# Performance work log

Hardware: AMD Instinct MI355X
Metric: run time of the kernel (lower is better)

Reference implementation:

```python
import jax, jax.numpy as jnp
import numpy as np

MARGIN = 0.3
N = 8192
D = 128
NUM_CLASSES = 256

def setup_inputs() -> dict:
    key = jax.random.key(0)
    k1, k2 = jax.random.split(key)
    inputs = jax.random.normal(k1, (N, D), dtype=jnp.float32)
    targets = jax.random.randint(k2, (N,), 0, NUM_CLASSES, dtype=jnp.int64)
    return {"inputs": inputs, "targets": targets}

def reference(inputs, targets):
    n = inputs.shape[0]
    dt = inputs.dtype
    # pairwise euclidean distances: ||xi||^2 + ||xj||^2 - 2 xi.xj, clamped and sqrt'ed
    sq = jnp.sum(inputs * inputs, axis=1)                     # [n]
    d2 = sq[:, None] + sq[None, :] - 2.0 * (inputs @ inputs.T)
    dist = jnp.sqrt(jnp.clip(d2, 1e-12, None))                # [n, n]
    dsq = dist * dist                                         # squared dists used by the loss

    mask = targets[:, None] == targets[None, :]               # same-identity mask [n, n]

    # positives: torch code sorts and drops the smallest (the self-distance ~1e-6)
    pos_d = jnp.where(mask, dist, jnp.inf)
    min_idx = jnp.argmin(pos_d, axis=1)                       # index of dropped element per row
    excl = jnp.arange(n)[None, :] == min_idx[:, None]
    pos_valid = mask & ~excl                                  # remaining positives
    cnt_p = jnp.sum(pos_valid, axis=1).astype(dt)
    sigma_p = jnp.sum(jnp.where(pos_valid, dsq, 0.0), axis=1) / cnt_p
    max_p = jnp.max(jnp.where(pos_valid, dsq, -jnp.inf), axis=1)
    dist_ap = max_p / sigma_p + 0.5 * jnp.log(sigma_p)        # [n]

    # negatives: all different-identity entries
    neg = ~mask
    cnt_n = jnp.sum(neg, axis=1).astype(dt)
    sigma_n = jnp.sum(jnp.where(neg, dsq, 0.0), axis=1) / cnt_n
    min_n = jnp.min(jnp.where(neg, dsq, jnp.inf), axis=1)
    dist_an = min_n / sigma_n + 0.5 * jnp.log(sigma_n)        # [n]

    # MarginRankingLoss with y=1: mean(max(0, -(an - ap) + margin))
    loss = jnp.mean(jnp.maximum(dist_ap - dist_an + MARGIN, 0.0))
    return loss
```

## Files before the change

kernel.cpp:

```cpp
#include <hip/hip_runtime.h>
#include <math.h>


#define NROWS 8192
#define MARGIN_F 0.3f

#define OFF_SQ   0
#define OFF_UPK  8192
#define OFF_XBF  16384
#define OFF_PART 540672

typedef short bf16x8 __attribute__((ext_vector_type(8)));
typedef float f32x16 __attribute__((ext_vector_type(16)));
union U4B { uint4 u; bf16x8 h; };

__device__ __forceinline__ unsigned short f2bf(float x) {
    unsigned u = __float_as_uint(x);
    return (unsigned short)((u + 0x7fffu + ((u >> 16) & 1u)) >> 16);
}

__global__ __launch_bounds__(256) void prep_kernel(const float* __restrict__ X,
                                                   const int* __restrict__ tgt,
                                                   float* __restrict__ sq,
                                                   float* __restrict__ upk,
                                                   unsigned short* __restrict__ Xbf,
                                                   float* __restrict__ out) {
    int tid = threadIdx.x, w = tid >> 6, l = tid & 63;
    #pragma unroll
    for (int i = 0; i < 4; ++i) {
        int r = blockIdx.x * 16 + w * 4 + i;
        float2 v = ((const float2*)X)[(size_t)r * 64 + l];
        ushort2 h2;
        h2.x = f2bf(v.x);
        h2.y = f2bf(v.y);
        ((ushort2*)Xbf)[(size_t)r * 64 + l] = h2;
        float s = v.x * v.x + v.y * v.y;
        for (int d = 32; d > 0; d >>= 1) s += __shfl_down(s, d, 64);
        if (l == 0) {
            sq[r] = s;
            upk[r] = __uint_as_float((__float_as_uint(0.5f * s) & 0xffffff00u)
                                     | (unsigned)tgt[r]);
        }
    }
    if (blockIdx.x == 0 && tid == 0) out[0] = 0.0f;
}

__global__ __launch_bounds__(256, 4) void dist_kernel(
        const unsigned short* __restrict__ Xbf, const int* __restrict__ tgt,
        const float* __restrict__ upk, float4* __restrict__ partial,
        int ns_mask, int jb_shift, int tiles) {
    __shared__ uint4 As[128 * 16];
    __shared__ float ush[128];
    const int tid = threadIdx.x;
    const int w = tid >> 6, l = tid & 63, hl = l >> 5, l31 = l & 31;
    const int bx = blockIdx.x;
    const int slice = bx & ns_mask;
    const int jb = bx >> jb_shift;

    {
        const uint4* src = (const uint4*)Xbf + (size_t)jb * 64 * 16;
        #pragma unroll
        for (int s = 0; s < 4; ++s) {
            int g = s * 256 + tid, row = g >> 4, c = g & 15;
            As[row * 16 + (c ^ (row & 15))] = src[g];
        }
    }
    __syncthreads();
    bf16x8 Bf[2][8];
    int tjt[2];
    #pragma unroll
    for (int ct = 0; ct < 2; ++ct) {
        int colb = ct * 32 + l31;
        tjt[ct] = tgt[jb * 64 + colb];
        #pragma unroll
        for (int kk = 0; kk < 8; ++kk) {
            U4B t; t.u = As[colb * 16 + ((kk * 2 + hl) ^ (colb & 15))];
            Bf[ct][kk] = t.h;
        }
    }

    float Sa[2] = {0.f, 0.f};
    float Ss[2] = {0.f, 0.f};
    float Mp[2] = {-INFINITY, -INFINITY};
    float Mn[2] = { INFINITY,  INFINITY};

    for (int t = 0; t < tiles; ++t) {
        const int i0 = (slice * tiles + t) * 128;
        __syncthreads();
        {
            const uint4* src = (const uint4*)Xbf + (size_t)i0 * 16;
            #pragma unroll
            for (int s = 0; s < 8; ++s) {
                int g = s * 256 + tid, row = g >> 4, c = g & 15;
                As[row * 16 + (c ^ (row & 15))] = src[g];
            }
            if (tid < 128) ush[tid] = upk[i0 + tid];
        }
        __syncthreads();

        float ur[16];
        int tags[16];
        #pragma unroll
        for (int r = 0; r < 16; ++r) {
            ur[r] = ush[w * 32 + (r & 3) + 8 * (r >> 2) + 4 * hl];
            tags[r] = __float_as_int(ur[r]) & 0xff;
        }

        f32x16 acc[2];
        acc[0] = (f32x16)0.0f;
        acc[1] = (f32x16)0.0f;
        const int arow = w * 32 + l31;
        #pragma unroll
        for (int kk = 0; kk < 8; ++kk) {
            U4B a; a.u = As[arow * 16 + ((kk * 2 + hl) ^ (arow & 15))];
            acc[0] = __builtin_amdgcn_mfma_f32_32x32x16_bf16(a.h, Bf[0][kk], acc[0], 0, 0, 0);
            acc[1] = __builtin_amdgcn_mfma_f32_32x32x16_bf16(a.h, Bf[1][kk], acc[1], 0, 0, 0);
        }

        #pragma unroll
        for (int ct = 0; ct < 2; ++ct) {
            const int tt = tjt[ct];
            #pragma unroll
            for (int r = 0; r < 16; ++r) {
                float a = acc[ct][r];
                float v = ur[r] - a;
                bool same = (tags[r] == tt);
                Sa[ct] += a;
                Ss[ct] += same ? a : 0.0f;
                Mp[ct] = fmaxf(Mp[ct], same ? v : -INFINITY);
                Mn[ct] = same ? Mn[ct] : fminf(Mn[ct], v);
            }
        }
    }

    #pragma unroll
    for (int ct = 0; ct < 2; ++ct) {
        Sa[ct] += __shfl_xor(Sa[ct], 32, 64);
        Ss[ct] += __shfl_xor(Ss[ct], 32, 64);
        Mp[ct] = fmaxf(Mp[ct], __shfl_xor(Mp[ct], 32, 64));
        Mn[ct] = fminf(Mn[ct], __shfl_xor(Mn[ct], 32, 64));
    }
    __syncthreads();
    float4* sm = (float4*)As;
    if (l < 32) {
        #pragma unroll
        for (int ct = 0; ct < 2; ++ct)
            sm[(ct * 32 + l31) * 4 + w] = make_float4(Sa[ct], Ss[ct], Mp[ct], Mn[ct]);
    }
    __syncthreads();
    if (tid < 64) {
        float4 a = sm[tid * 4 + 0], b = sm[tid * 4 + 1];
        float4 c2 = sm[tid * 4 + 2], d = sm[tid * 4 + 3];
        float4 o;
        o.x = a.x + b.x + c2.x + d.x;
        o.y = a.y + b.y + c2.y + d.y;
        o.z = fmaxf(fmaxf(a.z, b.z), fmaxf(c2.z, d.z));
        o.w = fminf(fminf(a.w, b.w), fminf(c2.w, d.w));
        partial[(size_t)slice * NROWS + jb * 64 + tid] = o;
    }
}

__global__ __launch_bounds__(256) void combine_kernel(
        const int* __restrict__ tgt, const float* __restrict__ sq,
        const float4* __restrict__ partial, float* __restrict__ out, int ns) {
    __shared__ float scl[256];
    __shared__ int cnt[256];
    __shared__ float red[4];
    __shared__ float hs[4];
    int tid = threadIdx.x, w = tid >> 6, l = tid & 63;
    scl[tid] = 0.0f;
    cnt[tid] = 0;
    __syncthreads();
    for (int it = 0; it < 32; ++it) {
        int r = it * 256 + tid;
        int c = tgt[r];
        atomicAdd(&scl[c], sq[r]);
        atomicAdd(&cnt[c], 1);
    }
    __syncthreads();
    float s = scl[tid];
    for (int d = 32; d > 0; d >>= 1) s += __shfl_down(s, d, 64);
    if (l == 0) red[w] = s;
    __syncthreads();
    float S_all = red[0] + red[1] + red[2] + red[3];

    int j = blockIdx.x * 256 + tid;
    float Sa = 0.f, Ss = 0.f, Mp = -INFINITY, Mn = INFINITY;
    for (int s2 = 0; s2 < ns; ++s2) {
        float4 p = partial[(size_t)s2 * NROWS + j];
        Sa += p.x; Ss += p.y;
        Mp = fmaxf(Mp, p.z); Mn = fminf(Mn, p.w);
    }
    float sqj = sq[j];
    int c = tgt[j];
    float cm = (float)cnt[c];
    float sumall = (float)NROWS * sqj + S_all - 2.0f * Sa;
    float sump = cm * sqj + scl[c] - 2.0f * Ss;
    float sumn = sumall - sump;
    float sigp = sump / (cm - 1.0f);
    float sign_ = sumn / ((float)NROWS - cm);
    float ap = (sqj + 2.0f * Mp) / sigp + 0.5f * __logf(sigp);
    float an = (sqj + 2.0f * Mn) / sign_ + 0.5f * __logf(sign_);
    float h = fmaxf(ap - an + MARGIN_F, 0.0f);
    for (int d = 32; d > 0; d >>= 1) h += __shfl_down(h, d, 64);
    if (l == 0) hs[w] = h;
    __syncthreads();
    if (tid == 0)
        atomicAdd(out, (hs[0] + hs[1] + hs[2] + hs[3]) * (1.0f / NROWS));
}

extern "C" void kernel_launch(void* const* d_in, const int* in_sizes, int n_in,
                              void* d_out, int out_size, void* d_ws, size_t ws_size,
                              hipStream_t stream) {
    const float* X = (const float*)d_in[0];
    const int* tgt = (const int*)d_in[1];
    float* out = (float*)d_out;
    float* f = (float*)d_ws;

    float* sq  = f + OFF_SQ;
    float* upk = f + OFF_UPK;
    unsigned short* Xbf = (unsigned short*)(f + OFF_XBF);
    float4* partial = (float4*)(f + OFF_PART);

    int ns = 16;
    while (ns > 2 && ws_size < ((size_t)OFF_PART + (size_t)ns * NROWS * 4) * sizeof(float))
        ns >>= 1;
    int shift = (ns == 16) ? 4 : (ns == 8) ? 3 : 2;
    int tiles = 64 / ns;

    prep_kernel<<<512, 256, 0, stream>>>(X, tgt, sq, upk, Xbf, out);
    dist_kernel<<<128 * ns, 256, 0, stream>>>(Xbf, tgt, upk, partial,
                                              ns - 1, shift, tiles);
    combine_kernel<<<32, 256, 0, stream>>>(tgt, sq, partial, out, ns);
}
```

Measured before the change: 120.4 us.

## Sort rows by class and compute distance sums algebraically outside the GEMM loop

Rows are counting-sorted by class label, so same-class entries form a contiguous band. The per-row sums of squared distances are computed separately from class-sum and global-sum vectors via dot products. This leaves the GEMM epilogue doing only the positive max and negative min, with a cheap min-only path for tiles that contain no same-class rows. It adds four small kernels (histogram, prefix offsets, scatter, class dots) plus extra launches and serial per-class work in exchange for a lighter epilogue and smaller partial output.

New measurement: 135.4 us. +12.4%, slower.

```diff
diff --git a/kernel.cpp b/kernel.cpp
--- a/kernel.cpp
+++ b/kernel.cpp
@@ -5,10 +5,22 @@
 #define NROWS 8192
 #define MARGIN_F 0.3f
 
-#define OFF_SQ   0
-#define OFF_UPK  8192
-#define OFF_XBF  16384
-#define OFF_PART 540672
+#define O_HIST   0
+#define O_OFF    256
+#define O_BOFF   512
+#define O_BH     16896
+#define O_PCS    33280
+#define O_PSQ    41472
+#define O_SVEC   41536
+#define O_SALL   41664
+#define O_SQ     41680
+#define O_US     49872
+#define O_CSA    58064
+#define O_WDA    66256
+#define O_SUMP   74448
+#define O_SUMALL 82640
+#define O_XS     90832
+#define O_PART   615120
 
 typedef short bf16x8 __attribute__((ext_vector_type(8)));
 typedef float f32x16 __attribute__((ext_vector_type(16)));
@@ -18,39 +30,193 @@
     unsigned u = __float_as_uint(x);
     return (unsigned short)((u + 0x7fffu + ((u >> 16) & 1u)) >> 16);
 }
+__device__ __forceinline__ float b2f(unsigned short h) {
+    return __uint_as_float(((unsigned)h) << 16);
+}
 
 __global__ __launch_bounds__(256) void prep_kernel(const float* __restrict__ X,
                                                    const int* __restrict__ tgt,
-                                                   float* __restrict__ sq,
-                                                   float* __restrict__ upk,
-                                                   unsigned short* __restrict__ Xbf,
-                                                   float* __restrict__ out) {
-    int tid = threadIdx.x, w = tid >> 6, l = tid & 63;
-    #pragma unroll
-    for (int i = 0; i < 4; ++i) {
-        int r = blockIdx.x * 16 + w * 4 + i;
+                                                   float* __restrict__ f) {
+    int*   bh  = (int*)(f + O_BH);
+    float* pcs = f + O_PCS;
+    float* psq = f + O_PSQ;
+    float* sq  = f + O_SQ;
+    __shared__ int lh[256];
+    __shared__ float csum[128];
+    __shared__ float ph[4];
+    int tid = threadIdx.x, w = tid >> 6, l = tid & 63, b = blockIdx.x;
+    int row0 = b * 128;
+    lh[tid] = 0;
+    __syncthreads();
+    if (tid < 128) atomicAdd(&lh[tgt[row0 + tid]], 1);
+    {
+        int d = tid & 127, r0 = (tid >> 7) * 64;
+        float a = 0.0f;
+        #pragma unroll 8
+        for (int r = 0; r < 64; ++r)
+            a += X[(size_t)(row0 + r0 + r) * 128 + d];
+        if (tid < 128) csum[tid] = a;
+        __syncthreads();
+        if (tid >= 128) csum[tid - 128] += a;
+        __syncthreads();
+        if (tid < 128) pcs[b * 128 + tid] = csum[tid];
+    }
+    float ss = 0.0f;
+    for (int i = 0; i < 32; ++i) {
+        int r = row0 + w * 32 + i;
         float2 v = ((const float2*)X)[(size_t)r * 64 + l];
+        float s = v.x * v.x + v.y * v.y;
+        for (int d = 32; d > 0; d >>= 1) s += __shfl_down(s, d, 64);
+        if (l == 0) { sq[r] = s; ss += s; }
+    }
+    if (l == 0) ph[w] = ss;
+    __syncthreads();
+    if (tid == 0) psq[b] = ph[0] + ph[1] + ph[2] + ph[3];
+    bh[b * 256 + tid] = lh[tid];
+}
+
+__global__ __launch_bounds__(256) void offsets_kernel(float* __restrict__ f,
+                                                      float* __restrict__ out) {
+    int*   hist = (int*)(f + O_HIST);
+    int*   off  = (int*)(f + O_OFF);
+    int*   boff = (int*)(f + O_BOFF);
+    int*   bh   = (int*)(f + O_BH);
+    float* pcs  = f + O_PCS;
+    float* psq  = f + O_PSQ;
+    float* svec = f + O_SVEC;
+    float* sall = f + O_SALL;
+    __shared__ int sh[256];
+    int c = threadIdx.x;
+    int h = 0;
+    for (int b = 0; b < 64; ++b) h += bh[b * 256 + c];
+    hist[c] = h;
+    sh[c] = h;
+    __syncthreads();
+    for (int d = 1; d < 256; d <<= 1) {
+        int t = (c >= d) ? sh[c - d] : 0;
+        __syncthreads();
+        sh[c] += t;
+        __syncthreads();
+    }
+    int o = sh[c] - h;
+    off[c] = o;
+    int run = o;
+    for (int b = 0; b < 64; ++b) {
+        boff[b * 256 + c] = run;
+        run += bh[b * 256 + c];
+    }
+    if (c < 128) {
+        float s = 0.0f;
+        for (int b = 0; b < 64; ++b) s += pcs[b * 128 + c];
+        svec[c] = s;
+    }
+    if (c < 64) {
+        float t = psq[c];
+        for (int d = 32; d > 0; d >>= 1) t += __shfl_down(t, d, 64);
+        if (c == 0) sall[0] = t;
+    }
+    if (c == 0) out[0] = 0.0f;
+}
+
+__global__ __launch_bounds__(256) void scatter_kernel(const float* __restrict__ X,
+                                                      const int* __restrict__ tgt,
+                                                      float* __restrict__ f) {
+    int*   hist = (int*)(f + O_HIST);
+    int*   off  = (int*)(f + O_OFF);
+    int*   boff = (int*)(f + O_BOFF);
+    float* sq   = f + O_SQ;
+    float* u_s  = f + O_US;
+    int*   csA  = (int*)(f + O_CSA);
+    int*   wdA  = (int*)(f + O_WDA);
+    unsigned short* Xs = (unsigned short*)(f + O_XS);
+    __shared__ int cur[256];
+    __shared__ int pos_sh[128];
+    int tid = threadIdx.x, b = blockIdx.x;
+    cur[tid] = boff[b * 256 + tid];
+    __syncthreads();
+    int row0 = b * 128;
+    if (tid < 128) {
+        int c = tgt[row0 + tid];
+        int p = atomicAdd(&cur[c], 1);
+        pos_sh[tid] = p;
+        u_s[p] = 0.5f * sq[row0 + tid];
+        csA[p] = off[c];
+        wdA[p] = hist[c];
+    }
+    __syncthreads();
+    int w = tid >> 6, l = tid & 63;
+    #pragma unroll 4
+    for (int i = 0; i < 32; ++i) {
+        int rl = w * 32 + i;
+        int p = pos_sh[rl];
+        float2 v = ((const float2*)X)[(size_t)(row0 + rl) * 64 + l];
         ushort2 h2;
         h2.x = f2bf(v.x);
         h2.y = f2bf(v.y);
-        ((ushort2*)Xbf)[(size_t)r * 64 + l] = h2;
-        float s = v.x * v.x + v.y * v.y;
-        for (int d = 32; d > 0; d >>= 1) s += __shfl_down(s, d, 64);
+        ((ushort2*)Xs)[(size_t)p * 64 + l] = h2;
+    }
+}
+
+__global__ __launch_bounds__(256) void classdot_kernel(float* __restrict__ f) {
+    int*   hist = (int*)(f + O_HIST);
+    int*   off  = (int*)(f + O_OFF);
+    float* svg  = f + O_SVEC;
+    float* sall = f + O_SALL;
+    float* u_s  = f + O_US;
+    float* sump_s   = f + O_SUMP;
+    float* sumall_s = f + O_SUMALL;
+    unsigned short* Xs = (unsigned short*)(f + O_XS);
+    __shared__ float sv[128];
+    __shared__ float cv[128];
+    __shared__ float sclsh;
+    int c = blockIdx.x, tid = threadIdx.x, w = tid >> 6, l = tid & 63;
+    int n = hist[c], cs0 = off[c];
+    if (tid < 128) sv[tid] = svg[tid];
+    {
+        int d = tid & 127;
+        float a = 0.0f;
+        for (int k = (tid >> 7); k < n; k += 2)
+            a += b2f(Xs[(size_t)(cs0 + k) * 128 + d]);
+        if (tid < 128) cv[tid] = a;
+        __syncthreads();
+        if (tid >= 128) cv[tid - 128] += a;
+    }
+    if (tid == 0) {
+        float s = 0.0f;
+        for (int k = 0; k < n; ++k) s += 2.0f * u_s[cs0 + k];
+        sclsh = s;
+    }
+    __syncthreads();
+    float Scl = sclsh, SA = sall[0];
+    for (int k = w; k < n; k += 4) {
+        int j = cs0 + k;
+        ushort2 xv = ((const ushort2*)Xs)[(size_t)j * 64 + l];
+        float x0 = b2f(xv.x), x1 = b2f(xv.y);
+        float pa = sv[2 * l] * x0 + sv[2 * l + 1] * x1;
+        float pb = cv[2 * l] * x0 + cv[2 * l + 1] * x1;
+        for (int d = 32; d > 0; d >>= 1) {
+            pa += __shfl_down(pa, d, 64);
+            pb += __shfl_down(pb, d, 64);
+        }
         if (l == 0) {
-            sq[r] = s;
-            upk[r] = __uint_as_float((__float_as_uint(0.5f * s) & 0xffffff00u)
-                                     | (unsigned)tgt[r]);
-        }
-    }
-    if (blockIdx.x == 0 && tid == 0) out[0] = 0.0f;
-}
-
-__global__ __launch_bounds__(256, 4) void dist_kernel(
-        const unsigned short* __restrict__ Xbf, const int* __restrict__ tgt,
-        const float* __restrict__ upk, float4* __restrict__ partial,
-        int ns_mask, int jb_shift, int tiles) {
+            float sqj = 2.0f * u_s[j];
+            sump_s[j]   = (float)n * sqj + Scl - 2.0f * pb;
+            sumall_s[j] = (float)NROWS * sqj + SA - 2.0f * pa;
+        }
+    }
+}
+
+__global__ __launch_bounds__(256, 3) void dist_kernel(float* __restrict__ f,
+                                                      int ns_mask, int jb_shift,
+                                                      int tiles) {
     __shared__ uint4 As[128 * 16];
     __shared__ float ush[128];
+    float* u_s = f + O_US;
+    int*   csA = (int*)(f + O_CSA);
+    int*   wdA = (int*)(f + O_WDA);
+    unsigned short* Xs = (unsigned short*)(f + O_XS);
+    float2* partial = (float2*)(f + O_PART);
+
     const int tid = threadIdx.x;
     const int w = tid >> 6, l = tid & 63, hl = l >> 5, l31 = l & 31;
     const int bx = blockIdx.x;
@@ -58,7 +224,7 @@
     const int jb = bx >> jb_shift;
 
     {
-        const uint4* src = (const uint4*)Xbf + (size_t)jb * 64 * 16;
+        const uint4* src = (const uint4*)Xs + (size_t)jb * 64 * 16;
         #pragma unroll
         for (int s = 0; s < 4; ++s) {
             int g = s * 256 + tid, row = g >> 4, c = g & 15;
@@ -67,11 +233,12 @@
     }
     __syncthreads();
     bf16x8 Bf[2][8];
-    int tjt[2];
+    int cs[2], wd[2];
     #pragma unroll
     for (int ct = 0; ct < 2; ++ct) {
         int colb = ct * 32 + l31;
-        tjt[ct] = tgt[jb * 64 + colb];
+        cs[ct] = csA[jb * 64 + colb];
+        wd[ct] = wdA[jb * 64 + colb];
         #pragma unroll
         for (int kk = 0; kk < 8; ++kk) {
             U4B t; t.u = As[colb * 16 + ((kk * 2 + hl) ^ (colb & 15))];
@@ -79,8 +246,6 @@
         }
     }
 
-    float Sa[2] = {0.f, 0.f};
-    float Ss[2] = {0.f, 0.f};
     float Mp[2] = {-INFINITY, -INFINITY};
     float Mn[2] = { INFINITY,  INFINITY};
 
@@ -88,22 +253,25 @@
         const int i0 = (slice * tiles + t) * 128;
         __syncthreads();
         {
-            const uint4* src = (const uint4*)Xbf + (size_t)i0 * 16;
+            const uint4* src = (const uint4*)Xs + (size_t)i0 * 16;
             #pragma unroll
             for (int s = 0; s < 8; ++s) {
                 int g = s * 256 + tid, row = g >> 4, c = g & 15;
                 As[row * 16 + (c ^ (row & 15))] = src[g];
             }
-            if (tid < 128) ush[tid] = upk[i0 + tid];
+            if (tid < 128) ush[tid] = u_s[i0 + tid];
         }
         __syncthreads();
 
         float ur[16];
-        int tags[16];
-        #pragma unroll
-        for (int r = 0; r < 16; ++r) {
-            ur[r] = ush[w * 32 + (r & 3) + 8 * (r >> 2) + 4 * hl];
-            tags[r] = __float_as_int(ur[r]) & 0xff;
+        {
+            const int base = w * 32 + 4 * hl;
+            #pragma unroll
+            for (int q = 0; q < 4; ++q) {
+                float4 uq = *(const float4*)&ush[base + 8 * q];
+                ur[4 * q + 0] = uq.x; ur[4 * q + 1] = uq.y;
+                ur[4 * q + 2] = uq.z; ur[4 * q + 3] = uq.w;
+            }
         }
 
         f32x16 acc[2];
@@ -119,86 +287,74 @@
 
         #pragma unroll
         for (int ct = 0; ct < 2; ++ct) {
-            const int tt = tjt[ct];
-            #pragma unroll
-            for (int r = 0; r < 16; ++r) {
-                float a = acc[ct][r];
-                float v = ur[r] - a;
-                bool same = (tags[r] == tt);
-                Sa[ct] += a;
-                Ss[ct] += same ? a : 0.0f;
-                Mp[ct] = fmaxf(Mp[ct], same ? v : -INFINITY);
-                Mn[ct] = same ? Mn[ct] : fminf(Mn[ct], v);
+            bool band = (cs[ct] < i0 + 128) && (cs[ct] + wd[ct] > i0);
+            if (__any(band)) {
+                int rowb = i0 + w * 32 + 4 * hl - cs[ct];
+                unsigned wdu = (unsigned)wd[ct];
+                #pragma unroll
+                for (int r = 0; r < 16; ++r) {
+                    float v = ur[r] - acc[ct][r];
+                    bool in = (unsigned)(rowb + (r & 3) + 8 * (r >> 2)) < wdu;
+                    Mp[ct] = fmaxf(Mp[ct], in ? v : -INFINITY);
+                    Mn[ct] = in ? Mn[ct] : fminf(Mn[ct], v);
+                }
+            } else {
+                #pragma unroll
+                for (int r = 0; r < 16; r += 2) {
+                    float v1 = ur[r] - acc[ct][r];
+                    float v2 = ur[r + 1] - acc[ct][r + 1];
+                    Mn[ct] = fminf(Mn[ct], fminf(v1, v2));
+                }
             }
         }
     }
 
     #pragma unroll
     for (int ct = 0; ct < 2; ++ct) {
-        Sa[ct] += __shfl_xor(Sa[ct], 32, 64);
-        Ss[ct] += __shfl_xor(Ss[ct], 32, 64);
         Mp[ct] = fmaxf(Mp[ct], __shfl_xor(Mp[ct], 32, 64));
         Mn[ct] = fminf(Mn[ct], __shfl_xor(Mn[ct], 32, 64));
     }
     __syncthreads();
-    float4* sm = (float4*)As;
+    float2* sm = (float2*)As;
     if (l < 32) {
         #pragma unroll
         for (int ct = 0; ct < 2; ++ct)
-            sm[(ct * 32 + l31) * 4 + w] = make_float4(Sa[ct], Ss[ct], Mp[ct], Mn[ct]);
+            sm[(ct * 32 + l31) * 4 + w] = make_float2(Mp[ct], Mn[ct]);
     }
     __syncthreads();
     if (tid < 64) {
-        float4 a = sm[tid * 4 + 0], b = sm[tid * 4 + 1];
-        float4 c2 = sm[tid * 4 + 2], d = sm[tid * 4 + 3];
-        float4 o;
-        o.x = a.x + b.x + c2.x + d.x;
-        o.y = a.y + b.y + c2.y + d.y;
-        o.z = fmaxf(fmaxf(a.z, b.z), fmaxf(c2.z, d.z));
-        o.w = fminf(fminf(a.w, b.w), fminf(c2.w, d.w));
+        float2 a = sm[tid * 4 + 0], b = sm[tid * 4 + 1];
+        float2 c2 = sm[tid * 4 + 2], d = sm[tid * 4 + 3];
+        float2 o;
+        o.x = fmaxf(fmaxf(a.x, b.x), fmaxf(c2.x, d.x));
+        o.y = fminf(fminf(a.y, b.y), fminf(c2.y, d.y));
         partial[(size_t)slice * NROWS + jb * 64 + tid] = o;
     }
 }
 
-__global__ __launch_bounds__(256) void combine_kernel(
-        const int* __restrict__ tgt, const float* __restrict__ sq,
-        const float4* __restrict__ partial, float* __restrict__ out, int ns) {
-    __shared__ float scl[256];
-    __shared__ int cnt[256];
-    __shared__ float red[4];
+__global__ __launch_bounds__(256) void combine_kernel(float* __restrict__ f,
+                                                      float* __restrict__ out,
+                                                      int ns) {
+    float* u_s = f + O_US;
+    int*   wdA = (int*)(f + O_WDA);
+    float* sump_s   = f + O_SUMP;
+    float* sumall_s = f + O_SUMALL;
+    float2* partial = (float2*)(f + O_PART);
     __shared__ float hs[4];
     int tid = threadIdx.x, w = tid >> 6, l = tid & 63;
-    scl[tid] = 0.0f;
-    cnt[tid] = 0;
-    __syncthreads();
-    for (int it = 0; it < 32; ++it) {
-        int r = it * 256 + tid;
-        int c = tgt[r];
-        atomicAdd(&scl[c], sq[r]);
-        atomicAdd(&cnt[c], 1);
-    }
-    __syncthreads();
-    float s = scl[tid];
-    for (int d = 32; d > 0; d >>= 1) s += __shfl_down(s, d, 64);
-    if (l == 0) red[w] = s;
-    __syncthreads();
-    float S_all = red[0] + red[1] + red[2] + red[3];
-
     int j = blockIdx.x * 256 + tid;
-    float Sa = 0.f, Ss = 0.f, Mp = -INFINITY, Mn = INFINITY;
-    for (int s2 = 0; s2 < ns; ++s2) {
-        float4 p = partial[(size_t)s2 * NROWS + j];
-        Sa += p.x; Ss += p.y;
-        Mp = fmaxf(Mp, p.z); Mn = fminf(Mn, p.w);
-    }
-    float sqj = sq[j];
-    int c = tgt[j];
-    float cm = (float)cnt[c];
-    float sumall = (float)NROWS * sqj + S_all - 2.0f * Sa;
-    float sump = cm * sqj + scl[c] - 2.0f * Ss;
-    float sumn = sumall - sump;
+    float Mp = -INFINITY, Mn = INFINITY;
+    for (int s = 0; s < ns; ++s) {
+        float2 p = partial[(size_t)s * NROWS + j];
+        Mp = fmaxf(Mp, p.x);
+        Mn = fminf(Mn, p.y);
+    }
+    float sqj = 2.0f * u_s[j];
+    float cm = (float)wdA[j];
+    float sump = sump_s[j];
+    float sumall = sumall_s[j];
     float sigp = sump / (cm - 1.0f);
-    float sign_ = sumn / ((float)NROWS - cm);
+    float sign_ = (sumall - sump) / ((float)NROWS - cm);
     float ap = (sqj + 2.0f * Mp) / sigp + 0.5f * __logf(sigp);
     float an = (sqj + 2.0f * Mn) / sign_ + 0.5f * __logf(sign_);
     float h = fmaxf(ap - an + MARGIN_F, 0.0f);
@@ -217,19 +373,16 @@
     float* out = (float*)d_out;
     float* f = (float*)d_ws;
 
-    float* sq  = f + OFF_SQ;
-    float* upk = f + OFF_UPK;
-    unsigned short* Xbf = (unsigned short*)(f + OFF_XBF);
-    float4* partial = (float4*)(f + OFF_PART);
-
     int ns = 16;
-    while (ns > 2 && ws_size < ((size_t)OFF_PART + (size_t)ns * NROWS * 4) * sizeof(float))
+    while (ns > 2 && ws_size < ((size_t)O_PART + (size_t)ns * NROWS * 2) * sizeof(float))
         ns >>= 1;
     int shift = (ns == 16) ? 4 : (ns == 8) ? 3 : 2;
     int tiles = 64 / ns;
 
-    prep_kernel<<<512, 256, 0, stream>>>(X, tgt, sq, upk, Xbf, out);
-    dist_kernel<<<128 * ns, 256, 0, stream>>>(Xbf, tgt, upk, partial,
-                                              ns - 1, shift, tiles);
-    combine_kernel<<<32, 256, 0, stream>>>(tgt, sq, partial, out, ns);
-}
+    prep_kernel<<<64, 256, 0, stream>>>(X, tgt, f);
+    offsets_kernel<<<1, 256, 0, stream>>>(f, out);
+    scatter_kernel<<<64, 256, 0, stream>>>(X, tgt, f);
+    classdot_kernel<<<256, 256, 0, stream>>>(f);
+    dist_kernel<<<128 * ns, 256, 0, stream>>>(f, ns - 1, shift, tiles);
+    combine_kernel<<<32, 256, 0, stream>>>(f, out, ns);
+}
```
